# Kernel tuning notes

Measured on AMD Instinct MI355X. Metric: run time of the kernel, lower is better.

Reference implementation:

```python
import jax, jax.numpy as jnp
import numpy as np

N_NODES = 50000
N_EDGES = 1600000
N_DECODE = 500000
D = 128
EPS = 1e-6


def _sage_conv(x, src, dst, Wl, bl, Wr, n_nodes):
    # PyG SAGEConv (mean aggr): out = lin_l(mean_{j in N(i)} x_j) + lin_r(x_i)
    msg = x[src]                                            # [E, D] gather
    s = jax.ops.segment_sum(msg, dst, num_segments=n_nodes) # [N, D]
    cnt = jax.ops.segment_sum(jnp.ones((src.shape[0],), x.dtype), dst,
                              num_segments=n_nodes)         # [N]
    aggr = s / jnp.maximum(cnt, 1.0)[:, None]
    return aggr @ Wl + bl + x @ Wr


def setup_inputs() -> dict:
    key = jax.random.key(0)
    ks = jax.random.split(key, 9)
    scale = 1.0 / np.sqrt(D)
    x = jax.random.normal(ks[0], (N_NODES, D), dtype=jnp.float32)
    edge_index = jax.random.randint(ks[1], (2, N_EDGES), 0, N_NODES, dtype=jnp.int64)
    decode_index = jax.random.randint(ks[2], (2, N_DECODE), 0, N_NODES, dtype=jnp.int64)
    W1l = jax.random.normal(ks[3], (D, D), dtype=jnp.float32) * scale
    b1 = jnp.zeros((D,), dtype=jnp.float32)
    W1r = jax.random.normal(ks[4], (D, D), dtype=jnp.float32) * scale
    W2l = jax.random.normal(ks[5], (D, D), dtype=jnp.float32) * scale
    b2 = jnp.zeros((D,), dtype=jnp.float32)
    W2r = jax.random.normal(ks[6], (D, D), dtype=jnp.float32) * scale
    return {"x": x, "edge_index": edge_index, "decode_index": decode_index,
            "W1l": W1l, "b1": b1, "W1r": W1r, "W2l": W2l, "b2": b2, "W2r": W2r}


def reference(x, edge_index, decode_index, W1l, b1, W1r, W2l, b2, W2r):
    src, dst = edge_index[0], edge_index[1]
    h = _sage_conv(x, src, dst, W1l, b1, W1r, N_NODES)
    h = jax.nn.relu(h)
    # dropout is a no-op in eval mode (training=False)
    h = _sage_conv(h, src, dst, W2l, b2, W2r, N_NODES)
    a = h[decode_index[0]]                                  # [Dk, D]
    b = h[decode_index[1]]
    num = jnp.sum(a * b, axis=1)
    denom = jnp.maximum(jnp.linalg.norm(a, axis=1) * jnp.linalg.norm(b, axis=1), EPS)
    return jax.nn.sigmoid(num / denom)
```

## Files before the change

### kernel.cpp

```cpp
#include <hip/hip_runtime.h>
#include <cstddef>

#define D 128
#define NBITS 7
#define BCAP2 6144
#define CHUNK 4096
#define BSTRIDE8 36

typedef float floatx4 __attribute__((ext_vector_type(4)));
typedef float floatx2 __attribute__((ext_vector_type(2)));

__device__ __forceinline__ int incl_scan64(int v) {
    const int lane = threadIdx.x & 63;
#pragma unroll
    for (int o = 1; o < 64; o <<= 1) {
        int u = __shfl_up(v, o);
        if (lane >= o) v += u;
    }
    return v;
}

__device__ __forceinline__ void accf8p(floatx2* a2, uint4 u) {
    unsigned w[4] = {u.x, u.y, u.z, u.w};
#pragma unroll
    for (int k = 0; k < 4; ++k) {
        a2[2 * k + 0] += __builtin_amdgcn_cvt_pk_f32_fp8((int)w[k], false);
        a2[2 * k + 1] += __builtin_amdgcn_cvt_pk_f32_fp8((int)w[k], true);
    }
}

__device__ __forceinline__ float dotf8(uint4 ua, uint4 ub) {
    unsigned wa[4] = {ua.x, ua.y, ua.z, ua.w};
    unsigned wb[4] = {ub.x, ub.y, ub.z, ub.w};
    float dot = 0.f;
#pragma unroll
    for (int k = 0; k < 4; ++k) {
        floatx2 alo = __builtin_amdgcn_cvt_pk_f32_fp8((int)wa[k], false);
        floatx2 ahi = __builtin_amdgcn_cvt_pk_f32_fp8((int)wa[k], true);
        floatx2 blo = __builtin_amdgcn_cvt_pk_f32_fp8((int)wb[k], false);
        floatx2 bhi = __builtin_amdgcn_cvt_pk_f32_fp8((int)wb[k], true);
        dot = fmaf(alo.x, blo.x, dot);
        dot = fmaf(alo.y, blo.y, dot);
        dot = fmaf(ahi.x, bhi.x, dot);
        dot = fmaf(ahi.y, bhi.y, dot);
    }
    return dot;
}

__global__ void __launch_bounds__(256) k1_prep_bucket(
        const float* __restrict__ x, unsigned* __restrict__ xf8,
        int nq, int nblk_a,
        const float* __restrict__ W1l, const float* __restrict__ W1r,
        const float* __restrict__ W2l, const float* __restrict__ W2r,
        unsigned* __restrict__ Wtf8,
        const int* __restrict__ src, const int* __restrict__ dst, int n_edges,
        unsigned* __restrict__ chunk_data, int* __restrict__ chunk_off,
        int nbuck) {
    int blk = (int)blockIdx.x;
    const int tid = threadIdx.x;
    if (blk < nblk_a) {
        int t = blk * 256 + tid;
        if (t < nq) {
            float4 v = ((const float4*)x)[t];
            int lo = __builtin_amdgcn_cvt_pk_fp8_f32(v.x, v.y, 0, false);
            xf8[t] = (unsigned)__builtin_amdgcn_cvt_pk_fp8_f32(v.z, v.w, lo, true);
        }
        return;
    }
    blk -= nblk_a;
    if (blk < 64) {
        int t2 = blk * 256 + tid;
        int widx = t2 >> 12;
        int within = t2 & 4095;
        int n = within >> 5;
        int g = within & 31;
        const float* W = (widx == 0) ? W1l : (widx == 1) ? W1r : (widx == 2) ? W2l : W2r;
        float w0 = W[(size_t)(4 * g + 0) * D + n];
        float w1 = W[(size_t)(4 * g + 1) * D + n];
        float w2 = W[(size_t)(4 * g + 2) * D + n];
        float w3 = W[(size_t)(4 * g + 3) * D + n];
        int lo = __builtin_amdgcn_cvt_pk_fp8_f32(w0, w1, 0, false);
        Wtf8[(size_t)widx * 4096 + (size_t)n * 32 + g] =
            (unsigned)__builtin_amdgcn_cvt_pk_fp8_f32(w2, w3, lo, true);
        return;
    }
    blk -= 64;
    __shared__ int cnt[512];
    __shared__ int cur[512];
    __shared__ int wsum[4];
    __shared__ unsigned ent[CHUNK];
    const int c = blk;
    const int e0 = c * CHUNK;
    const int n = min(CHUNK, n_edges - e0);
    cnt[tid] = 0;
    cnt[tid + 256] = 0;
    __syncthreads();
    for (int i = tid; i < n; i += 256)
        atomicAdd(&cnt[dst[e0 + i] >> NBITS], 1);
    __syncthreads();
    int c0 = cnt[2 * tid], c1 = cnt[2 * tid + 1];
    int v = c0 + c1;
    int s = incl_scan64(v);
    if ((tid & 63) == 63) wsum[tid >> 6] = s;
    __syncthreads();
    {
        int wv = tid >> 6;
        int add = (wv > 0 ? wsum[0] : 0) + (wv > 1 ? wsum[1] : 0) + (wv > 2 ? wsum[2] : 0);
        int excl = s + add - v;
        cur[2 * tid] = excl;
        cur[2 * tid + 1] = excl + c0;
        const int stride = nbuck + 1;
        if (2 * tid <= nbuck) chunk_off[(size_t)c * stride + 2 * tid] = excl;
        if (2 * tid + 1 <= nbuck) chunk_off[(size_t)c * stride + 2 * tid + 1] = excl + c0;
    }
    __syncthreads();
    for (int i = tid; i < n; i += 256) {
        int d = dst[e0 + i];
        int sv = src[e0 + i];
        int b = d >> NBITS;
        int p = atomicAdd(&cur[b], 1);
        ent[p] = ((unsigned)(d & ((1 << NBITS) - 1)) << 16) | (unsigned)sv;
    }
    __syncthreads();
    for (int i = tid; i < n; i += 256) chunk_data[(size_t)e0 + i] = ent[i];
}

__global__ void __launch_bounds__(512, 4) k2_layer1(
        const unsigned* __restrict__ chunk_data, const int* __restrict__ chunk_off,
        int nchunk, int nbuck,
        const unsigned* __restrict__ xf8, const unsigned* __restrict__ Wt,
        const float* __restrict__ bias,
        unsigned* __restrict__ csr16g, int* __restrict__ offsG,
        unsigned* __restrict__ aggf8, unsigned char* __restrict__ h1,
        int n_nodes) {
    __shared__ unsigned sB[2][128 * BSTRIDE8];
    __shared__ unsigned short lcsr[BCAP2];
    __shared__ int ndeg[128], ncur[128], offs_l[130];
    __shared__ int s_w0;
    const int tid = threadIdx.x;
    const int b = blockIdx.x;
    const int stride = nbuck + 1;

    if (tid < 128) ndeg[tid] = 0;
    __syncthreads();

    const int w = tid >> 1, half = tid & 1;
    for (int c = w; c < nchunk; c += 256) {
        int beg = chunk_off[(size_t)c * stride + b];
        int end = chunk_off[(size_t)c * stride + b + 1];
        const unsigned* cd = chunk_data + (size_t)c * CHUNK;
        for (int i = beg + half; i < end; i += 2)
            atomicAdd(&ndeg[cd[i] >> 16], 1);
    }
    __syncthreads();
    int v = 0, s = 0;
    if (tid < 128) {
        v = ndeg[tid];
        s = incl_scan64(v);
        if (tid == 63) s_w0 = s;
    }
    __syncthreads();
    if (tid < 128) {
        if (tid >= 64) s += s_w0;
        int excl = min(s - v, BCAP2);
        ncur[tid] = excl;
        offs_l[tid] = excl;
        offsG[(size_t)b * 129 + tid] = excl;
        if (tid == 127) {
            int tot = min(s, BCAP2);
            offs_l[128] = tot;
            offsG[(size_t)b * 129 + 128] = tot;
        }
    }
    __syncthreads();
    for (int c = w; c < nchunk; c += 256) {
        int beg = chunk_off[(size_t)c * stride + b];
        int end = chunk_off[(size_t)c * stride + b + 1];
        const unsigned* cd = chunk_data + (size_t)c * CHUNK;
        for (int i = beg + half; i < end; i += 2) {
            unsigned e = cd[i];
            int pos = atomicAdd(&ncur[e >> 16], 1);
            if (pos < BCAP2) lcsr[pos] = (unsigned short)(e & 0xffffu);
        }
    }
    for (int i = tid; i < 2048; i += 512) {
        int m = i >> 10;
        int col = (i >> 3) & 127;
        int c4 = (i & 7) * 4;
        *(uint4*)&sB[m][col * BSTRIDE8 + c4] =
            *(const uint4*)(Wt + (size_t)m * 4096 + (size_t)col * 32 + c4);
    }
    __syncthreads();
    {
        int tot = offs_l[128];
        int words = (tot + 1) >> 1;
        const unsigned* l32 = (const unsigned*)lcsr;
        for (int i = tid; i < words; i += 512)
            csr16g[(size_t)b * (BCAP2 / 2) + i] = l32[i];
    }
    const int wv2 = tid >> 6;
    const int lane = tid & 63;
    const int q = lane >> 3;
    const int l8 = lane & 7;
    const unsigned* fb = xf8 + (size_t)l8 * 4;
#pragma unroll
    for (int pass = 0; pass < 2; ++pass) {
        const int nl = pass * 64 + wv2 * 8 + q;
        const int beg = offs_l[nl];
        const int end = offs_l[nl + 1];
        floatx2 a2[8];
#pragma unroll
        for (int i = 0; i < 8; ++i) a2[i] = (floatx2)(0.f);
        int e = beg;
        for (; e + 2 <= end; e += 2) {
            int s0 = lcsr[e];
            int s1 = lcsr[e + 1];
            uint4 u0 = *(const uint4*)(fb + (size_t)s0 * 32);
            uint4 u1 = *(const uint4*)(fb + (size_t)s1 * 32);
            accf8p(a2, u0);
            accf8p(a2, u1);
        }
        if (e < end) {
            int s0 = lcsr[e];
            uint4 u0 = *(const uint4*)(fb + (size_t)s0 * 32);
            accf8p(a2, u0);
        }
        float r = 1.0f / fmaxf((float)(end - beg), 1.0f);
        unsigned o[4];
#pragma unroll
        for (int j = 0; j < 4; ++j) {
            int lo = __builtin_amdgcn_cvt_pk_fp8_f32(a2[2 * j].x * r, a2[2 * j].y * r, 0, false);
            o[j] = (unsigned)__builtin_amdgcn_cvt_pk_fp8_f32(a2[2 * j + 1].x * r,
                                                             a2[2 * j + 1].y * r, lo, true);
        }
        const int node = b * 128 + nl;
        if (node < n_nodes)
            *(uint4*)(aggf8 + (size_t)node * 32 + l8 * 4) = make_uint4(o[0], o[1], o[2], o[3]);
    }
    __syncthreads();

    const int li = lane & 15;
    const int quad = lane >> 4;
    const int node0 = b * 128 + wv2 * 16;
    if (node0 >= n_nodes) return;

    floatx4 acc[8];
#pragma unroll
    for (int t = 0; t < 8; ++t) acc[t] = (floatx4)(0.f);

    int arow = node0 + li;
    if (arow >= n_nodes) arow = n_nodes - 1;
    const unsigned* aptr1 = aggf8 + (size_t)arow * 32 + quad * 2;
    const unsigned* aptr2 = xf8 + (size_t)arow * 32 + quad * 2;
    const unsigned* sb0 = &sB[0][li * BSTRIDE8 + quad * 2];
    const unsigned* sb1 = &sB[1][li * BSTRIDE8 + quad * 2];

#pragma unroll
    for (int ks = 0; ks < 4; ++ks) {
        long af = *(const long*)(aptr1 + ks * 8);
#pragma unroll
        for (int ct = 0; ct < 8; ++ct) {
            long bf = *(const long*)(sb0 + ct * 16 * BSTRIDE8 + ks * 8);
            acc[ct] = __builtin_amdgcn_mfma_f32_16x16x32_fp8_fp8(af, bf, acc[ct], 0, 0, 0);
        }
    }
#pragma unroll
    for (int ks = 0; ks < 4; ++ks) {
        long af = *(const long*)(aptr2 + ks * 8);
#pragma unroll
        for (int ct = 0; ct < 8; ++ct) {
            long bf = *(const long*)(sb1 + ct * 16 * BSTRIDE8 + ks * 8);
            acc[ct] = __builtin_amdgcn_mfma_f32_16x16x32_fp8_fp8(af, bf, acc[ct], 0, 0, 0);
        }
    }
#pragma unroll
    for (int ct = 0; ct < 8; ++ct) {
        int col = ct * 16 + li;
        float bv = bias[col];
#pragma unroll
        for (int r = 0; r < 4; ++r) {
            int node = node0 + quad * 4 + r;
            float o = acc[ct][r] + bv;
            o = fmaxf(o, 0.f);
            int pk = __builtin_amdgcn_cvt_pk_fp8_f32(o, o, 0, false);
            if (node < n_nodes)
                h1[(size_t)node * D + col] = (unsigned char)(pk & 0xff);
        }
    }
}

__global__ void __launch_bounds__(512, 4) k3_layer2(
        const int* __restrict__ offsG, const unsigned* __restrict__ csr16g,
        const unsigned* __restrict__ h1f8, const unsigned* __restrict__ Wt2,
        const float* __restrict__ bias,
        unsigned* __restrict__ aggf8, unsigned char* __restrict__ h2,
        float* __restrict__ nrm2, int n_nodes) {
    __shared__ unsigned sB[2][128 * BSTRIDE8];
    __shared__ int offs_l[130];
    const int tid = threadIdx.x;
    const int b = blockIdx.x;
    if (tid < 129) offs_l[tid] = offsG[(size_t)b * 129 + tid];
    for (int i = tid; i < 2048; i += 512) {
        int m = i >> 10;
        int col = (i >> 3) & 127;
        int c4 = (i & 7) * 4;
        *(uint4*)&sB[m][col * BSTRIDE8 + c4] =
            *(const uint4*)(Wt2 + (size_t)m * 4096 + (size_t)col * 32 + c4);
    }
    __syncthreads();

    const unsigned short* csr = (const unsigned short*)csr16g + (size_t)b * BCAP2;
    const int wv2 = tid >> 6;
    const int lane = tid & 63;
    const int q = lane >> 3;
    const int l8 = lane & 7;
    const unsigned* fb = h1f8 + (size_t)l8 * 4;
#pragma unroll
    for (int pass = 0; pass < 2; ++pass) {
        const int nl = pass * 64 + wv2 * 8 + q;
        const int beg = offs_l[nl];
        const int end = offs_l[nl + 1];
        floatx2 a2[8];
#pragma unroll
        for (int i = 0; i < 8; ++i) a2[i] = (floatx2)(0.f);
        int e = beg;
        for (; e + 2 <= end; e += 2) {
            int s0 = csr[e];
            int s1 = csr[e + 1];
            uint4 u0 = *(const uint4*)(fb + (size_t)s0 * 32);
            uint4 u1 = *(const uint4*)(fb + (size_t)s1 * 32);
            accf8p(a2, u0);
            accf8p(a2, u1);
        }
        if (e < end) {
            int s0 = csr[e];
            uint4 u0 = *(const uint4*)(fb + (size_t)s0 * 32);
            accf8p(a2, u0);
        }
        float r = 1.0f / fmaxf((float)(end - beg), 1.0f);
        unsigned o[4];
#pragma unroll
        for (int j = 0; j < 4; ++j) {
            int lo = __builtin_amdgcn_cvt_pk_fp8_f32(a2[2 * j].x * r, a2[2 * j].y * r, 0, false);
            o[j] = (unsigned)__builtin_amdgcn_cvt_pk_fp8_f32(a2[2 * j + 1].x * r,
                                                             a2[2 * j + 1].y * r, lo, true);
        }
        const int node = b * 128 + nl;
        if (node < n_nodes)
            *(uint4*)(aggf8 + (size_t)node * 32 + l8 * 4) = make_uint4(o[0], o[1], o[2], o[3]);
    }
    __syncthreads();

    const int li = lane & 15;
    const int quad = lane >> 4;
    const int node0 = b * 128 + wv2 * 16;
    if (node0 >= n_nodes) return;

    floatx4 acc[8];
#pragma unroll
    for (int t = 0; t < 8; ++t) acc[t] = (floatx4)(0.f);

    int arow = node0 + li;
    if (arow >= n_nodes) arow = n_nodes - 1;
    const unsigned* aptr1 = aggf8 + (size_t)arow * 32 + quad * 2;
    const unsigned* aptr2 = h1f8 + (size_t)arow * 32 + quad * 2;
    const unsigned* sb0 = &sB[0][li * BSTRIDE8 + quad * 2];
    const unsigned* sb1 = &sB[1][li * BSTRIDE8 + quad * 2];

#pragma unroll
    for (int ks = 0; ks < 4; ++ks) {
        long af = *(const long*)(aptr1 + ks * 8);
#pragma unroll
        for (int ct = 0; ct < 8; ++ct) {
            long bf = *(const long*)(sb0 + ct * 16 * BSTRIDE8 + ks * 8);
            acc[ct] = __builtin_amdgcn_mfma_f32_16x16x32_fp8_fp8(af, bf, acc[ct], 0, 0, 0);
        }
    }
#pragma unroll
    for (int ks = 0; ks < 4; ++ks) {
        long af = *(const long*)(aptr2 + ks * 8);
#pragma unroll
        for (int ct = 0; ct < 8; ++ct) {
            long bf = *(const long*)(sb1 + ct * 16 * BSTRIDE8 + ks * 8);
            acc[ct] = __builtin_amdgcn_mfma_f32_16x16x32_fp8_fp8(af, bf, acc[ct], 0, 0, 0);
        }
    }
    float sq[4] = {0.f, 0.f, 0.f, 0.f};
#pragma unroll
    for (int ct = 0; ct < 8; ++ct) {
        int col = ct * 16 + li;
        float bv = bias[col];
#pragma unroll
        for (int r = 0; r < 4; ++r) {
            int node = node0 + quad * 4 + r;
            float o = acc[ct][r] + bv;
            int pk = __builtin_amdgcn_cvt_pk_fp8_f32(o, o, 0, false);
            floatx2 dq = __builtin_amdgcn_cvt_pk_f32_fp8(pk, false);
            sq[r] += dq.x * dq.x;
            if (node < n_nodes)
                h2[(size_t)node * D + col] = (unsigned char)(pk & 0xff);
        }
    }
#pragma unroll
    for (int r = 0; r < 4; ++r) {
        float sv = sq[r];
        sv += __shfl_xor(sv, 1);
        sv += __shfl_xor(sv, 2);
        sv += __shfl_xor(sv, 4);
        sv += __shfl_xor(sv, 8);
        int node = node0 + quad * 4 + r;
        if (li == 0 && node < n_nodes) nrm2[node] = sv;
    }
}

__global__ void decode_kernel(const unsigned* __restrict__ h8, const float* __restrict__ nrm2,
                              const int* __restrict__ ia, const int* __restrict__ ib,
                              float* __restrict__ out, int n_pairs) {
    int t = blockIdx.x * blockDim.x + threadIdx.x;
    int p = t >> 3;
    if (p >= n_pairs) return;
    int l8 = t & 7;
    int i0 = ia[p];
    int i1 = ib[p];
    uint4 ua = *(const uint4*)(h8 + (size_t)i0 * 32 + l8 * 4);
    uint4 ub = *(const uint4*)(h8 + (size_t)i1 * 32 + l8 * 4);
    float dot = dotf8(ua, ub);
    dot += __shfl_xor(dot, 1);
    dot += __shfl_xor(dot, 2);
    dot += __shfl_xor(dot, 4);
    if (l8 == 0) {
        float denom = fmaxf(sqrtf(nrm2[i0] * nrm2[i1]), 1e-6f);
        float s = dot / denom;
        out[p] = 1.0f / (1.0f + expf(-s));
    }
}


extern "C" void kernel_launch(void* const* d_in, const int* in_sizes, int n_in,
                              void* d_out, int out_size, void* d_ws, size_t ws_size,
                              hipStream_t stream) {
    const float* x   = (const float*)d_in[0];
    const int*   ei  = (const int*)d_in[1];
    const int*   di  = (const int*)d_in[2];
    const float* W1l = (const float*)d_in[3];
    const float* b1  = (const float*)d_in[4];
    const float* W1r = (const float*)d_in[5];
    const float* W2l = (const float*)d_in[6];
    const float* b2  = (const float*)d_in[7];
    const float* W2r = (const float*)d_in[8];

    const int N = in_sizes[0] / D;
    const int E = in_sizes[1] / 2;
    const int K = in_sizes[2] / 2;
    const size_t NQ = (size_t)N * (D / 4);
    const int NBUCK = (N + (1 << NBITS) - 1) >> NBITS;
    const int NCHUNK = (E + CHUNK - 1) / CHUNK;

    const int* src  = ei;
    const int* dstp = ei + E;
    const int* dia  = di;
    const int* dib  = di + K;

    unsigned* ws         = (unsigned*)d_ws;
    unsigned* chunk_data = ws;
    int*      chunk_off  = (int*)(chunk_data + E);
    unsigned* csr16g     = (unsigned*)(chunk_off + (size_t)NCHUNK * (NBUCK + 1));
    int*      offsG      = (int*)(csr16g + (size_t)NBUCK * (BCAP2 / 2));
    float*    nrm2       = (float*)(offsG + (size_t)NBUCK * 129);
    unsigned* Wtf8       = (unsigned*)(nrm2 + N);
    unsigned* xf8        = Wtf8 + 16384;
    unsigned* h1f8       = xf8 + NQ;
    unsigned* h2f8       = h1f8 + NQ;
    unsigned* aggf8      = h2f8 + NQ;

    float* out = (float*)d_out;

    const int nq = (int)NQ;
    const int nblk_a = (nq + 255) / 256;

    k1_prep_bucket<<<nblk_a + 64 + NCHUNK, 256, 0, stream>>>(
        x, xf8, nq, nblk_a, W1l, W1r, W2l, W2r, Wtf8,
        src, dstp, E, chunk_data, chunk_off, NBUCK);

    k2_layer1<<<NBUCK, 512, 0, stream>>>(
        chunk_data, chunk_off, NCHUNK, NBUCK, xf8, Wtf8, b1,
        csr16g, offsG, aggf8, (unsigned char*)h1f8, N);

    k3_layer2<<<NBUCK, 512, 0, stream>>>(
        offsG, csr16g, h1f8, Wtf8 + 8192, b2,
        aggf8, (unsigned char*)h2f8, nrm2, N);

    {
        long long threads = (long long)K * 8;
        int blocks = (int)((threads + 255) / 256);
        decode_kernel<<<blocks, 256, 0, stream>>>(h2f8, nrm2, dia, dib, out, K);
    }
}
```

Before: 232.9 us.

## Split fp8 feature rows into two 64-byte planes and halve bucket size

Stores node features (x, h1, h2, agg) as two separate 64-column planes, so each plane pass of the gather touches a smaller working set that fits in cache better. Buckets shrink from 128 to 64 nodes with 256-thread blocks, which doubles the block count for the layer kernels. Gather loops are unrolled by four, and decode handles eight pairs per thread split across the two planes. In exchange each gathered row is fetched in two passes over the edge list, and chunk_off doubles in size.

```diff
diff --git a/kernel.cpp b/kernel.cpp
--- a/kernel.cpp
+++ b/kernel.cpp
@@ -2,10 +2,11 @@
 #include <cstddef>
 
 #define D 128
-#define NBITS 7
-#define BCAP2 6144
+#define NBITS 6
+#define BCAP2 3072
 #define CHUNK 4096
 #define BSTRIDE8 36
+#define DNPP 8
 
 typedef float floatx4 __attribute__((ext_vector_type(4)));
 typedef float floatx2 __attribute__((ext_vector_type(2)));
@@ -49,7 +50,7 @@
 
 __global__ void __launch_bounds__(256) k1_prep_bucket(
         const float* __restrict__ x, unsigned* __restrict__ xf8,
-        int nq, int nblk_a,
+        int nq, int nblk_a, int N16,
         const float* __restrict__ W1l, const float* __restrict__ W1r,
         const float* __restrict__ W2l, const float* __restrict__ W2r,
         unsigned* __restrict__ Wtf8,
@@ -63,7 +64,9 @@
         if (t < nq) {
             float4 v = ((const float4*)x)[t];
             int lo = __builtin_amdgcn_cvt_pk_fp8_f32(v.x, v.y, 0, false);
-            xf8[t] = (unsigned)__builtin_amdgcn_cvt_pk_fp8_f32(v.z, v.w, lo, true);
+            unsigned w = (unsigned)__builtin_amdgcn_cvt_pk_fp8_f32(v.z, v.w, lo, true);
+            int n = t >> 5, j = t & 31;
+            xf8[(size_t)(j >> 4) * N16 + (size_t)n * 16 + (j & 15)] = w;
         }
         return;
     }
@@ -85,33 +88,35 @@
         return;
     }
     blk -= 64;
-    __shared__ int cnt[512];
-    __shared__ int cur[512];
+    __shared__ int cnt[1024];
+    __shared__ int cur[1024];
     __shared__ int wsum[4];
     __shared__ unsigned ent[CHUNK];
     const int c = blk;
     const int e0 = c * CHUNK;
     const int n = min(CHUNK, n_edges - e0);
-    cnt[tid] = 0;
-    cnt[tid + 256] = 0;
+    *(int4*)&cnt[4 * tid] = make_int4(0, 0, 0, 0);
     __syncthreads();
     for (int i = tid; i < n; i += 256)
         atomicAdd(&cnt[dst[e0 + i] >> NBITS], 1);
     __syncthreads();
-    int c0 = cnt[2 * tid], c1 = cnt[2 * tid + 1];
-    int v = c0 + c1;
+    int4 cc = *(const int4*)&cnt[4 * tid];
+    int v = cc.x + cc.y + cc.z + cc.w;
     int s = incl_scan64(v);
     if ((tid & 63) == 63) wsum[tid >> 6] = s;
     __syncthreads();
     {
         int wv = tid >> 6;
         int add = (wv > 0 ? wsum[0] : 0) + (wv > 1 ? wsum[1] : 0) + (wv > 2 ? wsum[2] : 0);
-        int excl = s + add - v;
-        cur[2 * tid] = excl;
-        cur[2 * tid + 1] = excl + c0;
-        const int stride = nbuck + 1;
-        if (2 * tid <= nbuck) chunk_off[(size_t)c * stride + 2 * tid] = excl;
-        if (2 * tid + 1 <= nbuck) chunk_off[(size_t)c * stride + 2 * tid + 1] = excl + c0;
+        int ex = s + add - v;
+        int e1 = ex + cc.x, e2 = e1 + cc.y, e3 = e2 + cc.z;
+        cur[4 * tid] = ex; cur[4 * tid + 1] = e1;
+        cur[4 * tid + 2] = e2; cur[4 * tid + 3] = e3;
+        const size_t base = (size_t)c * (nbuck + 1);
+        if (4 * tid     <= nbuck) chunk_off[base + 4 * tid]     = ex;
+        if (4 * tid + 1 <= nbuck) chunk_off[base + 4 * tid + 1] = e1;
+        if (4 * tid + 2 <= nbuck) chunk_off[base + 4 * tid + 2] = e2;
+        if (4 * tid + 3 <= nbuck) chunk_off[base + 4 * tid + 3] = e3;
     }
     __syncthreads();
     for (int i = tid; i < n; i += 256) {
@@ -125,27 +130,26 @@
     for (int i = tid; i < n; i += 256) chunk_data[(size_t)e0 + i] = ent[i];
 }
 
-__global__ void __launch_bounds__(512, 4) k2_layer1(
+__global__ void __launch_bounds__(256, 3) k2_layer1(
         const unsigned* __restrict__ chunk_data, const int* __restrict__ chunk_off,
         int nchunk, int nbuck,
         const unsigned* __restrict__ xf8, const unsigned* __restrict__ Wt,
         const float* __restrict__ bias,
         unsigned* __restrict__ csr16g, int* __restrict__ offsG,
         unsigned* __restrict__ aggf8, unsigned char* __restrict__ h1,
-        int n_nodes) {
+        int n_nodes, int N16) {
     __shared__ unsigned sB[2][128 * BSTRIDE8];
     __shared__ unsigned short lcsr[BCAP2];
-    __shared__ int ndeg[128], ncur[128], offs_l[130];
-    __shared__ int s_w0;
+    __shared__ int ndeg[64], ncur[64], offs_l[65];
     const int tid = threadIdx.x;
     const int b = blockIdx.x;
     const int stride = nbuck + 1;
 
-    if (tid < 128) ndeg[tid] = 0;
+    if (tid < 64) ndeg[tid] = 0;
     __syncthreads();
 
     const int w = tid >> 1, half = tid & 1;
-    for (int c = w; c < nchunk; c += 256) {
+    for (int c = w; c < nchunk; c += 128) {
         int beg = chunk_off[(size_t)c * stride + b];
         int end = chunk_off[(size_t)c * stride + b + 1];
         const unsigned* cd = chunk_data + (size_t)c * CHUNK;
@@ -153,27 +157,21 @@
             atomicAdd(&ndeg[cd[i] >> 16], 1);
     }
     __syncthreads();
-    int v = 0, s = 0;
-    if (tid < 128) {
-        v = ndeg[tid];
-        s = incl_scan64(v);
-        if (tid == 63) s_w0 = s;
-    }
-    __syncthreads();
-    if (tid < 128) {
-        if (tid >= 64) s += s_w0;
+    if (tid < 64) {
+        int v = ndeg[tid];
+        int s = incl_scan64(v);
         int excl = min(s - v, BCAP2);
         ncur[tid] = excl;
         offs_l[tid] = excl;
-        offsG[(size_t)b * 129 + tid] = excl;
-        if (tid == 127) {
+        offsG[(size_t)b * 65 + tid] = excl;
+        if (tid == 63) {
             int tot = min(s, BCAP2);
-            offs_l[128] = tot;
-            offsG[(size_t)b * 129 + 128] = tot;
-        }
-    }
-    __syncthreads();
-    for (int c = w; c < nchunk; c += 256) {
+            offs_l[64] = tot;
+            offsG[(size_t)b * 65 + 64] = tot;
+        }
+    }
+    __syncthreads();
+    for (int c = w; c < nchunk; c += 128) {
         int beg = chunk_off[(size_t)c * stride + b];
         int end = chunk_off[(size_t)c * stride + b + 1];
         const unsigned* cd = chunk_data + (size_t)c * CHUNK;
@@ -183,7 +181,7 @@
             if (pos < BCAP2) lcsr[pos] = (unsigned short)(e & 0xffffu);
         }
     }
-    for (int i = tid; i < 2048; i += 512) {
+    for (int i = tid; i < 2048; i += 256) {
         int m = i >> 10;
         int col = (i >> 3) & 127;
         int c4 = (i & 7) * 4;
@@ -192,40 +190,47 @@
     }
     __syncthreads();
     {
-        int tot = offs_l[128];
+        int tot = offs_l[64];
         int words = (tot + 1) >> 1;
         const unsigned* l32 = (const unsigned*)lcsr;
-        for (int i = tid; i < words; i += 512)
+        for (int i = tid; i < words; i += 256)
             csr16g[(size_t)b * (BCAP2 / 2) + i] = l32[i];
     }
     const int wv2 = tid >> 6;
     const int lane = tid & 63;
-    const int q = lane >> 3;
-    const int l8 = lane & 7;
-    const unsigned* fb = xf8 + (size_t)l8 * 4;
-#pragma unroll
-    for (int pass = 0; pass < 2; ++pass) {
-        const int nl = pass * 64 + wv2 * 8 + q;
-        const int beg = offs_l[nl];
-        const int end = offs_l[nl + 1];
+    const int q = lane >> 2;
+    const int l4 = lane & 3;
+    const int nl = wv2 * 16 + q;
+    const int node = b * 64 + nl;
+    const int beg = offs_l[nl];
+    const int end = offs_l[nl + 1];
+    const float r = 1.0f / fmaxf((float)(end - beg), 1.0f);
+#pragma unroll
+    for (int plane = 0; plane < 2; ++plane) {
+        const unsigned* fb = xf8 + (size_t)plane * N16 + (size_t)l4 * 4;
         floatx2 a2[8];
 #pragma unroll
         for (int i = 0; i < 8; ++i) a2[i] = (floatx2)(0.f);
         int e = beg;
+        for (; e + 4 <= end; e += 4) {
+            int s0 = lcsr[e], s1 = lcsr[e + 1], s2 = lcsr[e + 2], s3 = lcsr[e + 3];
+            uint4 u0 = *(const uint4*)(fb + (size_t)s0 * 16);
+            uint4 u1 = *(const uint4*)(fb + (size_t)s1 * 16);
+            uint4 u2 = *(const uint4*)(fb + (size_t)s2 * 16);
+            uint4 u3 = *(const uint4*)(fb + (size_t)s3 * 16);
+            accf8p(a2, u0); accf8p(a2, u1); accf8p(a2, u2); accf8p(a2, u3);
+        }
         for (; e + 2 <= end; e += 2) {
-            int s0 = lcsr[e];
-            int s1 = lcsr[e + 1];
-            uint4 u0 = *(const uint4*)(fb + (size_t)s0 * 32);
-            uint4 u1 = *(const uint4*)(fb + (size_t)s1 * 32);
-            accf8p(a2, u0);
-            accf8p(a2, u1);
+            int s0 = lcsr[e], s1 = lcsr[e + 1];
+            uint4 u0 = *(const uint4*)(fb + (size_t)s0 * 16);
+            uint4 u1 = *(const uint4*)(fb + (size_t)s1 * 16);
+            accf8p(a2, u0); accf8p(a2, u1);
         }
         if (e < end) {
             int s0 = lcsr[e];
-            uint4 u0 = *(const uint4*)(fb + (size_t)s0 * 32);
+            uint4 u0 = *(const uint4*)(fb + (size_t)s0 * 16);
             accf8p(a2, u0);
         }
-        float r = 1.0f / fmaxf((float)(end - beg), 1.0f);
         unsigned o[4];
 #pragma unroll
         for (int j = 0; j < 4; ++j) {
@@ -233,15 +238,15 @@
             o[j] = (unsigned)__builtin_amdgcn_cvt_pk_fp8_f32(a2[2 * j + 1].x * r,
                                                              a2[2 * j + 1].y * r, lo, true);
         }
-        const int node = b * 128 + nl;
         if (node < n_nodes)
-            *(uint4*)(aggf8 + (size_t)node * 32 + l8 * 4) = make_uint4(o[0], o[1], o[2], o[3]);
+            *(uint4*)(aggf8 + (size_t)plane * N16 + (size_t)node * 16 + l4 * 4) =
+                make_uint4(o[0], o[1], o[2], o[3]);
     }
     __syncthreads();
 
     const int li = lane & 15;
     const int quad = lane >> 4;
-    const int node0 = b * 128 + wv2 * 16;
+    const int node0 = b * 64 + wv2 * 16;
     if (node0 >= n_nodes) return;
 
     floatx4 acc[8];
@@ -250,14 +255,14 @@
 
     int arow = node0 + li;
     if (arow >= n_nodes) arow = n_nodes - 1;
-    const unsigned* aptr1 = aggf8 + (size_t)arow * 32 + quad * 2;
-    const unsigned* aptr2 = xf8 + (size_t)arow * 32 + quad * 2;
+    const unsigned* ap = aggf8 + (size_t)arow * 16 + quad * 2;
+    const unsigned* xp = xf8 + (size_t)arow * 16 + quad * 2;
     const unsigned* sb0 = &sB[0][li * BSTRIDE8 + quad * 2];
     const unsigned* sb1 = &sB[1][li * BSTRIDE8 + quad * 2];
 
 #pragma unroll
     for (int ks = 0; ks < 4; ++ks) {
-        long af = *(const long*)(aptr1 + ks * 8);
+        long af = *(const long*)(ap + (size_t)(ks >> 1) * N16 + (ks & 1) * 8);
 #pragma unroll
         for (int ct = 0; ct < 8; ++ct) {
             long bf = *(const long*)(sb0 + ct * 16 * BSTRIDE8 + ks * 8);
@@ -266,7 +271,7 @@
     }
 #pragma unroll
     for (int ks = 0; ks < 4; ++ks) {
-        long af = *(const long*)(aptr2 + ks * 8);
+        long af = *(const long*)(xp + (size_t)(ks >> 1) * N16 + (ks & 1) * 8);
 #pragma unroll
         for (int ct = 0; ct < 8; ++ct) {
             long bf = *(const long*)(sb1 + ct * 16 * BSTRIDE8 + ks * 8);
@@ -277,30 +282,31 @@
     for (int ct = 0; ct < 8; ++ct) {
         int col = ct * 16 + li;
         float bv = bias[col];
-#pragma unroll
-        for (int r = 0; r < 4; ++r) {
-            int node = node0 + quad * 4 + r;
-            float o = acc[ct][r] + bv;
+        unsigned char* hp = h1 + (size_t)(col >> 6) * ((size_t)N16 * 4) + (col & 63);
+#pragma unroll
+        for (int r2 = 0; r2 < 4; ++r2) {
+            int node2 = node0 + quad * 4 + r2;
+            float o = acc[ct][r2] + bv;
             o = fmaxf(o, 0.f);
             int pk = __builtin_amdgcn_cvt_pk_fp8_f32(o, o, 0, false);
-            if (node < n_nodes)
-                h1[(size_t)node * D + col] = (unsigned char)(pk & 0xff);
-        }
-    }
-}
-
-__global__ void __launch_bounds__(512, 4) k3_layer2(
+            if (node2 < n_nodes)
+                hp[(size_t)node2 * 64] = (unsigned char)(pk & 0xff);
+        }
+    }
+}
+
+__global__ void __launch_bounds__(256, 3) k3_layer2(
         const int* __restrict__ offsG, const unsigned* __restrict__ csr16g,
         const unsigned* __restrict__ h1f8, const unsigned* __restrict__ Wt2,
         const float* __restrict__ bias,
         unsigned* __restrict__ aggf8, unsigned char* __restrict__ h2,
-        float* __restrict__ nrm2, int n_nodes) {
+        float* __restrict__ nrm2, int n_nodes, int N16) {
     __shared__ unsigned sB[2][128 * BSTRIDE8];
-    __shared__ int offs_l[130];
+    __shared__ int offs_l[65];
     const int tid = threadIdx.x;
     const int b = blockIdx.x;
-    if (tid < 129) offs_l[tid] = offsG[(size_t)b * 129 + tid];
-    for (int i = tid; i < 2048; i += 512) {
+    if (tid < 65) offs_l[tid] = offsG[(size_t)b * 65 + tid];
+    for (int i = tid; i < 2048; i += 256) {
         int m = i >> 10;
         int col = (i >> 3) & 127;
         int c4 = (i & 7) * 4;
@@ -312,32 +318,39 @@
     const unsigned short* csr = (const unsigned short*)csr16g + (size_t)b * BCAP2;
     const int wv2 = tid >> 6;
     const int lane = tid & 63;
-    const int q = lane >> 3;
-    const int l8 = lane & 7;
-    const unsigned* fb = h1f8 + (size_t)l8 * 4;
-#pragma unroll
-    for (int pass = 0; pass < 2; ++pass) {
-        const int nl = pass * 64 + wv2 * 8 + q;
-        const int beg = offs_l[nl];
-        const int end = offs_l[nl + 1];
+    const int q = lane >> 2;
+    const int l4 = lane & 3;
+    const int nl = wv2 * 16 + q;
+    const int node = b * 64 + nl;
+    const int beg = offs_l[nl];
+    const int end = offs_l[nl + 1];
+    const float r = 1.0f / fmaxf((float)(end - beg), 1.0f);
+#pragma unroll
+    for (int plane = 0; plane < 2; ++plane) {
+        const unsigned* fb = h1f8 + (size_t)plane * N16 + (size_t)l4 * 4;
         floatx2 a2[8];
 #pragma unroll
         for (int i = 0; i < 8; ++i) a2[i] = (floatx2)(0.f);
         int e = beg;
+        for (; e + 4 <= end; e += 4) {
+            int s0 = csr[e], s1 = csr[e + 1], s2 = csr[e + 2], s3 = csr[e + 3];
+            uint4 u0 = *(const uint4*)(fb + (size_t)s0 * 16);
+            uint4 u1 = *(const uint4*)(fb + (size_t)s1 * 16);
+            uint4 u2 = *(const uint4*)(fb + (size_t)s2 * 16);
+            uint4 u3 = *(const uint4*)(fb + (size_t)s3 * 16);
+            accf8p(a2, u0); accf8p(a2, u1); accf8p(a2, u2); accf8p(a2, u3);
+        }
         for (; e + 2 <= end; e += 2) {
-            int s0 = csr[e];
-            int s1 = csr[e + 1];
-            uint4 u0 = *(const uint4*)(fb + (size_t)s0 * 32);
-            uint4 u1 = *(const uint4*)(fb + (size_t)s1 * 32);
-            accf8p(a2, u0);
-            accf8p(a2, u1);
+            int s0 = csr[e], s1 = csr[e + 1];
+            uint4 u0 = *(const uint4*)(fb + (size_t)s0 * 16);
+            uint4 u1 = *(const uint4*)(fb + (size_t)s1 * 16);
+            accf8p(a2, u0); accf8p(a2, u1);
         }
         if (e < end) {
             int s0 = csr[e];
-            uint4 u0 = *(const uint4*)(fb + (size_t)s0 * 32);
+            uint4 u0 = *(const uint4*)(fb + (size_t)s0 * 16);
             accf8p(a2, u0);
         }
-        float r = 1.0f / fmaxf((float)(end - beg), 1.0f);
         unsigned o[4];
 #pragma unroll
         for (int j = 0; j < 4; ++j) {
@@ -345,15 +358,15 @@
             o[j] = (unsigned)__builtin_amdgcn_cvt_pk_fp8_f32(a2[2 * j + 1].x * r,
                                                              a2[2 * j + 1].y * r, lo, true);
         }
-        const int node = b * 128 + nl;
         if (node < n_nodes)
-            *(uint4*)(aggf8 + (size_t)node * 32 + l8 * 4) = make_uint4(o[0], o[1], o[2], o[3]);
+            *(uint4*)(aggf8 + (size_t)plane * N16 + (size_t)node * 16 + l4 * 4) =
+                make_uint4(o[0], o[1], o[2], o[3]);
     }
     __syncthreads();
 
     const int li = lane & 15;
     const int quad = lane >> 4;
-    const int node0 = b * 128 + wv2 * 16;
+    const int node0 = b * 64 + wv2 * 16;
     if (node0 >= n_nodes) return;
 
     floatx4 acc[8];
@@ -362,14 +375,14 @@
 
     int arow = node0 + li;
     if (arow >= n_nodes) arow = n_nodes - 1;
-    const unsigned* aptr1 = aggf8 + (size_t)arow * 32 + quad * 2;
-    const unsigned* aptr2 = h1f8 + (size_t)arow * 32 + quad * 2;
+    const unsigned* ap = aggf8 + (size_t)arow * 16 + quad * 2;
+    const unsigned* xp = h1f8 + (size_t)arow * 16 + quad * 2;
     const unsigned* sb0 = &sB[0][li * BSTRIDE8 + quad * 2];
     const unsigned* sb1 = &sB[1][li * BSTRIDE8 + quad * 2];
 
 #pragma unroll
     for (int ks = 0; ks < 4; ++ks) {
-        long af = *(const long*)(aptr1 + ks * 8);
+        long af = *(const long*)(ap + (size_t)(ks >> 1) * N16 + (ks & 1) * 8);
 #pragma unroll
         for (int ct = 0; ct < 8; ++ct) {
             long bf = *(const long*)(sb0 + ct * 16 * BSTRIDE8 + ks * 8);
@@ -378,7 +391,7 @@
     }
 #pragma unroll
     for (int ks = 0; ks < 4; ++ks) {
-        long af = *(const long*)(aptr2 + ks * 8);
+        long af = *(const long*)(xp + (size_t)(ks >> 1) * N16 + (ks & 1) * 8);
 #pragma unroll
         for (int ct = 0; ct < 8; ++ct) {
             long bf = *(const long*)(sb1 + ct * 16 * BSTRIDE8 + ks * 8);
@@ -390,48 +403,72 @@
     for (int ct = 0; ct < 8; ++ct) {
         int col = ct * 16 + li;
         float bv = bias[col];
-#pragma unroll
-        for (int r = 0; r < 4; ++r) {
-            int node = node0 + quad * 4 + r;
-            float o = acc[ct][r] + bv;
+        unsigned char* hp = h2 + (size_t)(col >> 6) * ((size_t)N16 * 4) + (col & 63);
+#pragma unroll
+        for (int r2 = 0; r2 < 4; ++r2) {
+            int node2 = node0 + quad * 4 + r2;
+            float o = acc[ct][r2] + bv;
             int pk = __builtin_amdgcn_cvt_pk_fp8_f32(o, o, 0, false);
             floatx2 dq = __builtin_amdgcn_cvt_pk_f32_fp8(pk, false);
-            sq[r] += dq.x * dq.x;
-            if (node < n_nodes)
-                h2[(size_t)node * D + col] = (unsigned char)(pk & 0xff);
-        }
-    }
-#pragma unroll
-    for (int r = 0; r < 4; ++r) {
-        float sv = sq[r];
+            sq[r2] += dq.x * dq.x;
+            if (node2 < n_nodes)
+                hp[(size_t)node2 * 64] = (unsigned char)(pk & 0xff);
+        }
+    }
+#pragma unroll
+    for (int r2 = 0; r2 < 4; ++r2) {
+        float sv = sq[r2];
         sv += __shfl_xor(sv, 1);
         sv += __shfl_xor(sv, 2);
         sv += __shfl_xor(sv, 4);
         sv += __shfl_xor(sv, 8);
-        int node = node0 + quad * 4 + r;
-        if (li == 0 && node < n_nodes) nrm2[node] = sv;
-    }
-}
-
-__global__ void decode_kernel(const unsigned* __restrict__ h8, const float* __restrict__ nrm2,
-                              const int* __restrict__ ia, const int* __restrict__ ib,
-                              float* __restrict__ out, int n_pairs) {
-    int t = blockIdx.x * blockDim.x + threadIdx.x;
-    int p = t >> 3;
-    if (p >= n_pairs) return;
-    int l8 = t & 7;
-    int i0 = ia[p];
-    int i1 = ib[p];
-    uint4 ua = *(const uint4*)(h8 + (size_t)i0 * 32 + l8 * 4);
-    uint4 ub = *(const uint4*)(h8 + (size_t)i1 * 32 + l8 * 4);
-    float dot = dotf8(ua, ub);
-    dot += __shfl_xor(dot, 1);
-    dot += __shfl_xor(dot, 2);
-    dot += __shfl_xor(dot, 4);
-    if (l8 == 0) {
-        float denom = fmaxf(sqrtf(nrm2[i0] * nrm2[i1]), 1e-6f);
-        float s = dot / denom;
-        out[p] = 1.0f / (1.0f + expf(-s));
+        int node2 = node0 + quad * 4 + r2;
+        if (li == 0 && node2 < n_nodes) nrm2[node2] = sv;
+    }
+}
+
+__global__ void __launch_bounds__(256) decode_kernel(
+        const unsigned* __restrict__ h2, const float* __restrict__ nrm2,
+        const int* __restrict__ ia, const int* __restrict__ ib,
+        float* __restrict__ out, int n_pairs, int N16) {
+    const int tid = threadIdx.x;
+    const int l4 = tid & 3;
+    const int g = blockIdx.x * 64 + (tid >> 2);
+    const int strideP = gridDim.x * 64;
+    float dp[DNPP];
+    int pa[DNPP], pb[DNPP];
+#pragma unroll
+    for (int i = 0; i < DNPP; ++i) {
+        dp[i] = 0.f;
+        int p = g + i * strideP;
+        pa[i] = 0; pb[i] = 0;
+        if (p < n_pairs) { pa[i] = ia[p]; pb[i] = ib[p]; }
+    }
+#pragma unroll
+    for (int plane = 0; plane < 2; ++plane) {
+        const unsigned* hb = h2 + (size_t)plane * N16 + (size_t)l4 * 4;
+#pragma unroll
+        for (int i = 0; i < DNPP; ++i) {
+            int p = g + i * strideP;
+            if (p < n_pairs) {
+                uint4 ua = *(const uint4*)(hb + (size_t)pa[i] * 16);
+                uint4 ub = *(const uint4*)(hb + (size_t)pb[i] * 16);
+                dp[i] += dotf8(ua, ub);
+            }
+        }
+    }
+#pragma unroll
+    for (int i = 0; i < DNPP; ++i) {
+        int p = g + i * strideP;
+        if (p >= n_pairs) continue;
+        float dot = dp[i];
+        dot += __shfl_xor(dot, 1);
+        dot += __shfl_xor(dot, 2);
+        if (l4 == 0) {
+            float denom = fmaxf(sqrtf(nrm2[pa[i]] * nrm2[pb[i]]), 1e-6f);
+            float s = dot / denom;
+            out[p] = 1.0f / (1.0f + expf(-s));
+        }
     }
 }
 
@@ -452,7 +489,8 @@
     const int N = in_sizes[0] / D;
     const int E = in_sizes[1] / 2;
     const int K = in_sizes[2] / 2;
-    const size_t NQ = (size_t)N * (D / 4);
+    const int N16 = N * 16;
+    const size_t NQ = (size_t)N * 32;
     const int NBUCK = (N + (1 << NBITS) - 1) >> NBITS;
     const int NCHUNK = (E + CHUNK - 1) / CHUNK;
 
@@ -466,7 +504,7 @@
     int*      chunk_off  = (int*)(chunk_data + E);
     unsigned* csr16g     = (unsigned*)(chunk_off + (size_t)NCHUNK * (NBUCK + 1));
     int*      offsG      = (int*)(csr16g + (size_t)NBUCK * (BCAP2 / 2));
-    float*    nrm2       = (float*)(offsG + (size_t)NBUCK * 129);
+    float*    nrm2       = (float*)(offsG + (size_t)NBUCK * 65);
     unsigned* Wtf8       = (unsigned*)(nrm2 + N);
     unsigned* xf8        = Wtf8 + 16384;
     unsigned* h1f8       = xf8 + NQ;
@@ -479,20 +517,19 @@
     const int nblk_a = (nq + 255) / 256;
 
     k1_prep_bucket<<<nblk_a + 64 + NCHUNK, 256, 0, stream>>>(
-        x, xf8, nq, nblk_a, W1l, W1r, W2l, W2r, Wtf8,
+        x, xf8, nq, nblk_a, N16, W1l, W1r, W2l, W2r, Wtf8,
         src, dstp, E, chunk_data, chunk_off, NBUCK);
 
-    k2_layer1<<<NBUCK, 512, 0, stream>>>(
+    k2_layer1<<<NBUCK, 256, 0, stream>>>(
         chunk_data, chunk_off, NCHUNK, NBUCK, xf8, Wtf8, b1,
-        csr16g, offsG, aggf8, (unsigned char*)h1f8, N);
-
-    k3_layer2<<<NBUCK, 512, 0, stream>>>(
+        csr16g, offsG, aggf8, (unsigned char*)h1f8, N, N16);
+
+    k3_layer2<<<NBUCK, 256, 0, stream>>>(
         offsG, csr16g, h1f8, Wtf8 + 8192, b2,
-        aggf8, (unsigned char*)h2f8, nrm2, N);
+        aggf8, (unsigned char*)h2f8, nrm2, N, N16);
 
     {
-        long long threads = (long long)K * 8;
-        int blocks = (int)((threads + 255) / 256);
-        decode_kernel<<<blocks, 256, 0, stream>>>(h2f8, nrm2, dia, dib, out, K);
-    }
-}
+        int G = (K + 64 * DNPP - 1) / (64 * DNPP);
+        decode_kernel<<<G, 256, 0, stream>>>(h2f8, nrm2, dia, dib, out, K, N16);
+    }
+}
```

Result: slower. 257.4 us (+10.5%).
